# Kernel tuning notes

Hardware: AMD Instinct MI355X
Metric: run time of the kernel (lower is better)

Reference implementation:

```python
import jax, jax.numpy as jnp
import numpy as np

B, T, D, H, E = 8, 4096, 128, 4, 65536
O = D // H
NEG_SLOPE = 0.2

def setup_inputs() -> dict:
    key = jax.random.key(0)
    ks = jax.random.split(key, 5)
    s = 1.0 / np.sqrt(D)
    return {
        "x": jax.random.normal(ks[0], (B, T, D), jnp.float32),
        "edge_index": jax.random.randint(ks[1], (2, E), 0, T, jnp.int64),
        "W": jax.random.normal(ks[2], (D, H * O), jnp.float32) * s,
        "att_src": jax.random.normal(ks[3], (H, O), jnp.float32) * s,
        "att_dst": jax.random.normal(ks[4], (H, O), jnp.float32) * s,
        "bias": jnp.zeros((H * O,), jnp.float32),
    }

def reference(x, edge_index, W, att_src, att_dst, bias):
    b, t, d = x.shape
    N = b * t
    # linear projection of all nodes: [N, H, O]
    h = (x.reshape(N, d) @ W).reshape(N, H, O)
    # tile edge_index across batch with node offsets b_idx * t (matches repeat(1, b) + offsets)
    e = edge_index.shape[1]
    offsets = jnp.repeat(jnp.arange(b, dtype=edge_index.dtype), e) * t
    src = jnp.tile(edge_index[0], b) + offsets
    dst = jnp.tile(edge_index[1], b) + offsets
    # PyG GATConv default: add self loops over all N nodes
    loop = jnp.arange(N, dtype=edge_index.dtype)
    src = jnp.concatenate([src, loop])
    dst = jnp.concatenate([dst, loop])
    # per-node attention logits [N, H]
    a_src = jnp.sum(h * att_src, axis=-1)
    a_dst = jnp.sum(h * att_dst, axis=-1)
    # per-edge attention, softmax over incoming edges of each dst node
    alpha = jax.nn.leaky_relu(a_src[src] + a_dst[dst], NEG_SLOPE)  # [Et, H]
    amax = jax.ops.segment_max(jax.lax.stop_gradient(alpha), dst, num_segments=N)
    ealpha = jnp.exp(alpha - amax[dst])
    denom = jax.ops.segment_sum(ealpha, dst, num_segments=N)
    alpha = ealpha / (denom[dst] + 1e-16)
    # weighted scatter-aggregate of source features
    msg = h[src] * alpha[:, :, None]  # [Et, H, O]
    out = jax.ops.segment_sum(msg, dst, num_segments=N)  # [N, H, O]
    out = out.reshape(N, H * O) + bias
    return out.reshape(b, t, d)
```

## Files before the change

### kernel.cpp

```cpp
#include <hip/hip_runtime.h>

#define BATCH    8
#define T_LEN    4096
#define D_DIM    128
#define H_HEADS  4
#define O_DIM    32
#define E_EDGES  65536
#define N_NODES  (BATCH * T_LEN)
#define NEG_SLOPE 0.2f
#define ELLCAP   64
#define SPILLCAP 8192
#define GEMM_BLOCKS 512

typedef __attribute__((ext_vector_type(8))) short short8;
typedef __attribute__((ext_vector_type(4))) float f32x4;

__device__ __forceinline__ unsigned int bf16b(float f) {
    unsigned int u = __float_as_uint(f);
    u += 0x7FFFu + ((u >> 16) & 1u);
    return u >> 16;
}
__device__ __forceinline__ unsigned int bf16pack(float lo, float hi) {
    return bf16b(lo) | (bf16b(hi) << 16);
}
__device__ __forceinline__ float bf16f(unsigned short u) {
    return __uint_as_float((unsigned int)u << 16);
}

__device__ __forceinline__ int detect_shift(const int* ei, int tidx, int* s_sh) {
    if (tidx < 64) {
        const int nz = (ei[2 * tidx + 1] != 0) ? 1 : 0;
        const unsigned long long b = __ballot(nz);
        if (tidx == 0) *s_sh = (b == 0ull) ? 1 : 0;
    }
    __syncthreads();
    return *s_sh;
}

__launch_bounds__(256)
__global__ void prep_kernel(const float* __restrict__ W,
                            int* __restrict__ cnt,
                            unsigned short* __restrict__ WtG) {
    const int g = blockIdx.x * 256 + threadIdx.x;
    if (g < T_LEN + 1) cnt[g] = 0;
    const int i = g - 4352;
    if (i >= 0 && i < 128 * 128) {
        const int k   = i >> 7;
        const int col = i & 127;
        WtG[col * 128 + k] = (unsigned short)bf16b(W[k * 128 + col]);
    }
}

__launch_bounds__(256)
__global__ void gemm_ell_kernel(const float* __restrict__ x,
                                const unsigned short* __restrict__ WtG,
                                const float* __restrict__ attS,
                                const float* __restrict__ attD,
                                const int* __restrict__ ei,
                                unsigned short* __restrict__ hb,
                                float* __restrict__ aS,
                                float* __restrict__ aD,
                                int* __restrict__ cnt,
                                int* __restrict__ ell,
                                int* __restrict__ spill_cnt,
                                int2* __restrict__ spill) {
    __shared__ short Xb[64][136];
    __shared__ short Wt[128][136];
    __shared__ int   s_sh;

    const int tid = threadIdx.x;

    if (blockIdx.x >= GEMM_BLOCKS) {
        const int sh = detect_shift(ei, tid, &s_sh);
        const int j  = (blockIdx.x - GEMM_BLOCKS) * 256 + tid;
        const int s  = ei[j << sh];
        const int d  = ei[(E_EDGES + j) << sh];
        const int p  = atomicAdd(&cnt[d], 1);
        if (p < ELLCAP) {
            ell[d * ELLCAP + p] = s;
        } else {
            const int q = atomicAdd(spill_cnt, 1);
            if (q < SPILLCAP) spill[q] = make_int2(s, d);
        }
        return;
    }

    const int row0 = (blockIdx.x & 7) * T_LEN + ((blockIdx.x >> 3) << 6);

    const float4* X4 = (const float4*)(x + (size_t)row0 * 128);
    #pragma unroll
    for (int i = 0; i < 8; ++i) {
        const int idx = tid + 256 * i;
        const int row = idx >> 5;
        const int c4  = (idx & 31) * 4;
        const float4 v = X4[idx];
        uint2 u;
        u.x = bf16pack(v.x, v.y);
        u.y = bf16pack(v.z, v.w);
        *(uint2*)&Xb[row][c4] = u;
    }

    #pragma unroll
    for (int i = 0; i < 8; ++i) {
        const int idx = tid + 256 * i;
        const int row = idx >> 4;
        const int off = (idx & 15) * 8;
        *(short8*)&Wt[row][off] = *(const short8*)&WtG[row * 128 + off];
    }
    __syncthreads();

    const int wv    = tid >> 6;
    const int l     = tid & 63;
    const int lr    = l & 15;
    const int lg    = l >> 4;
    const int wrow0 = wv * 16;

    f32x4 acc[8];
    #pragma unroll
    for (int cf = 0; cf < 8; ++cf) acc[cf] = (f32x4){0.f, 0.f, 0.f, 0.f};

    #pragma unroll
    for (int kt = 0; kt < 4; ++kt) {
        const int k0 = kt * 32 + lg * 8;
        const short8 a = *(const short8*)&Xb[wrow0 + lr][k0];
        #pragma unroll
        for (int cf = 0; cf < 8; ++cf) {
            const short8 b = *(const short8*)&Wt[cf * 16 + lr][k0];
            acc[cf] = __builtin_amdgcn_mfma_f32_16x16x32_bf16(a, b, acc[cf], 0, 0, 0);
        }
    }

    #pragma unroll
    for (int cf = 0; cf < 8; ++cf) {
        #pragma unroll
        for (int r = 0; r < 4; ++r) {
            const int row = row0 + wrow0 + lg * 4 + r;
            hb[(size_t)row * 128 + cf * 16 + lr] = (unsigned short)bf16b(acc[cf][r]);
        }
    }

    float psr[4][4];
    float pdr[4][4];
    #pragma unroll
    for (int r = 0; r < 4; ++r)
        #pragma unroll
        for (int hd = 0; hd < 4; ++hd) { psr[r][hd] = 0.f; pdr[r][hd] = 0.f; }

    #pragma unroll
    for (int cf = 0; cf < 8; ++cf) {
        const float aSc = attS[cf * 16 + lr];
        const float aDc = attD[cf * 16 + lr];
        const int   hd  = cf >> 1;
        #pragma unroll
        for (int r = 0; r < 4; ++r) {
            psr[r][hd] += acc[cf][r] * aSc;
            pdr[r][hd] += acc[cf][r] * aDc;
        }
    }
    #pragma unroll
    for (int r = 0; r < 4; ++r)
        #pragma unroll
        for (int hd = 0; hd < 4; ++hd)
            #pragma unroll
            for (int off = 1; off < 16; off <<= 1) {
                psr[r][hd] += __shfl_xor(psr[r][hd], off);
                pdr[r][hd] += __shfl_xor(pdr[r][hd], off);
            }
    if (lr == 0) {
        #pragma unroll
        for (int r = 0; r < 4; ++r) {
            const int row = row0 + wrow0 + lg * 4 + r;
            *(float4*)&aS[(size_t)row * 4] =
                make_float4(psr[r][0], psr[r][1], psr[r][2], psr[r][3]);
            *(float4*)&aD[(size_t)row * 4] =
                make_float4(pdr[r][0], pdr[r][1], pdr[r][2], pdr[r][3]);
        }
    }
}

__launch_bounds__(256)
__global__ void gather_kernel(const int* __restrict__ cnt,
                              const int* __restrict__ ell,
                              const int* __restrict__ spill_cnt,
                              const int2* __restrict__ spill,
                              const unsigned short* __restrict__ hb,
                              const float* __restrict__ aS,
                              const float* __restrict__ aD,
                              const float* __restrict__ bias,
                              float* __restrict__ out) {
    __shared__ int   sbuf[4][ELLCAP + 1];
    __shared__ float wbuf[4][ELLCAP + 1][4];

    const int batch = blockIdx.x & 7;
    const int wv    = threadIdx.x >> 6;
    const int nib   = ((blockIdx.x >> 3) << 2) + wv;
    const int lane  = threadIdx.x & 63;
    const int base  = batch * T_LEN;
    const int n     = base + nib;

    const int deg = cnt[nib];
    const int m   = (deg < ELLCAP) ? deg : ELLCAP;

    const float4 ad4 = *(const float4*)(aD + (size_t)n * 4);

    if (lane < m) {
        const int s = ell[nib * ELLCAP + lane] + base;
        const float4 as4 = *(const float4*)(aS + (size_t)s * 4);
        float4 l;
        l.x = as4.x + ad4.x; l.x = (l.x > 0.f) ? l.x : NEG_SLOPE * l.x;
        l.y = as4.y + ad4.y; l.y = (l.y > 0.f) ? l.y : NEG_SLOPE * l.y;
        l.z = as4.z + ad4.z; l.z = (l.z > 0.f) ? l.z : NEG_SLOPE * l.z;
        l.w = as4.w + ad4.w; l.w = (l.w > 0.f) ? l.w : NEG_SLOPE * l.w;
        sbuf[wv][lane]    = s;
        wbuf[wv][lane][0] = __expf(l.x);
        wbuf[wv][lane][1] = __expf(l.y);
        wbuf[wv][lane][2] = __expf(l.z);
        wbuf[wv][lane][3] = __expf(l.w);
    }
    if (lane == (m & 63)) {
        const float4 as4 = *(const float4*)(aS + (size_t)n * 4);
        float4 l;
        l.x = as4.x + ad4.x; l.x = (l.x > 0.f) ? l.x : NEG_SLOPE * l.x;
        l.y = as4.y + ad4.y; l.y = (l.y > 0.f) ? l.y : NEG_SLOPE * l.y;
        l.z = as4.z + ad4.z; l.z = (l.z > 0.f) ? l.z : NEG_SLOPE * l.z;
        l.w = as4.w + ad4.w; l.w = (l.w > 0.f) ? l.w : NEG_SLOPE * l.w;
        sbuf[wv][m]    = n;
        wbuf[wv][m][0] = __expf(l.x);
        wbuf[wv][m][1] = __expf(l.y);
        wbuf[wv][m][2] = __expf(l.z);
        wbuf[wv][m][3] = __expf(l.w);
    }

    const int half = lane >> 5;
    const int li   = lane & 31;
    const int ci   = li * 4;
    const int hh   = li >> 3;

    float4 A = make_float4(0.f, 0.f, 0.f, 0.f);
    float dsum = 0.f;
    const int nst = m + 1;
    #pragma unroll 4
    for (int j = half; j < nst; j += 2) {
        const int   s = sbuf[wv][j];
        const float w = wbuf[wv][j][hh];
        dsum += w;
        const ushort4 hv = *(const ushort4*)(hb + (size_t)s * 128 + ci);
        A.x += w * bf16f(hv.x);
        A.y += w * bf16f(hv.y);
        A.z += w * bf16f(hv.z);
        A.w += w * bf16f(hv.w);
    }

    int sc = *spill_cnt;
    if (sc > 0 && half == 0) {
        if (sc > SPILLCAP) sc = SPILLCAP;
        const float adh = aD[(size_t)n * 4 + hh];
        for (int q = 0; q < sc; ++q) {
            const int2 e = spill[q];
            if (e.y == nib) {
                const int s = e.x + base;
                float l = aS[(size_t)s * 4 + hh] + adh;
                l = (l > 0.f) ? l : NEG_SLOPE * l;
                const float w = __expf(l);
                dsum += w;
                const ushort4 hv = *(const ushort4*)(hb + (size_t)s * 128 + ci);
                A.x += w * bf16f(hv.x);
                A.y += w * bf16f(hv.y);
                A.z += w * bf16f(hv.z);
                A.w += w * bf16f(hv.w);
            }
        }
    }

    A.x += __shfl_xor(A.x, 32);
    A.y += __shfl_xor(A.y, 32);
    A.z += __shfl_xor(A.z, 32);
    A.w += __shfl_xor(A.w, 32);
    dsum += __shfl_xor(dsum, 32);

    if (half == 0) {
        const float inv = 1.0f / (dsum + 1e-16f);
        const float4 b = *(const float4*)(bias + ci);
        float4 o;
        o.x = A.x * inv + b.x;
        o.y = A.y * inv + b.y;
        o.z = A.z * inv + b.z;
        o.w = A.w * inv + b.w;
        *(float4*)(out + (size_t)n * 128 + ci) = o;
    }
}

extern "C" void kernel_launch(void* const* d_in, const int* in_sizes, int n_in,
                              void* d_out, int out_size, void* d_ws, size_t ws_size,
                              hipStream_t stream) {
    const float* x    = (const float*)d_in[0];
    const int*   ei   = (const int*)  d_in[1];
    const float* W    = (const float*)d_in[2];
    const float* attS = (const float*)d_in[3];
    const float* attD = (const float*)d_in[4];
    const float* bias = (const float*)d_in[5];
    float* out = (float*)d_out;

    float* ws = (float*)d_ws;
    unsigned short* hb  = (unsigned short*)ws;
    float* aS           = ws + (size_t)N_NODES * 64;
    float* aD           = aS + (size_t)N_NODES * 4;
    unsigned short* WtG = (unsigned short*)(aD + (size_t)N_NODES * 4);
    int*   cnt          = (int*)(WtG + 128 * 128);
    int*   spill_cnt    = cnt + T_LEN;
    int*   ell          = spill_cnt + 2;
    int2*  spill        = (int2*)(ell + T_LEN * ELLCAP);

    prep_kernel<<<81, 256, 0, stream>>>(W, cnt, WtG);

    gemm_ell_kernel<<<GEMM_BLOCKS + 256, 256, 0, stream>>>(
        x, WtG, attS, attD, ei, hb, aS, aD, cnt, ell, spill_cnt, spill);

    gather_kernel<<<N_NODES / 4, 256, 0, stream>>>(cnt, ell, spill_cnt, spill,
                                                   hb, aS, aD, bias, out);
}
```

Before: 42.62 us.

## Map one destination node per half-wave in gather kernel with 1024-thread blocks

The gather kernel now assigns each 32-lane half-wave its own destination node, so a 64-lane wave handles two nodes instead of splitting one node's edges across its halves. This removes the cross-half shuffle reduction and the idle half during the output store. Blocks grow to 1024 threads covering 32 nodes each. Each half-wave now loops over all of its node's edges serially, and edge-weight setup loops in steps of 32. Divergence between the two nodes in a wave, and the larger block's shared memory and register limits, may reduce occupancy.

Measured after the change: 40.81 us. 1.04x faster.

```diff
diff --git a/kernel.cpp b/kernel.cpp
--- a/kernel.cpp
+++ b/kernel.cpp
@@ -178,7 +178,7 @@
     }
 }
 
-__launch_bounds__(256)
+__launch_bounds__(1024)
 __global__ void gather_kernel(const int* __restrict__ cnt,
                               const int* __restrict__ ell,
                               const int* __restrict__ spill_cnt,
@@ -188,14 +188,16 @@
                               const float* __restrict__ aD,
                               const float* __restrict__ bias,
                               float* __restrict__ out) {
-    __shared__ int   sbuf[4][ELLCAP + 1];
-    __shared__ float wbuf[4][ELLCAP + 1][4];
+    __shared__ int   sbuf[16][2][ELLCAP + 1];
+    __shared__ float wbuf[16][2][ELLCAP + 1][4];
 
     const int batch = blockIdx.x & 7;
     const int wv    = threadIdx.x >> 6;
-    const int nib   = ((blockIdx.x >> 3) << 2) + wv;
     const int lane  = threadIdx.x & 63;
+    const int half  = lane >> 5;
+    const int li    = lane & 31;
     const int base  = batch * T_LEN;
+    const int nib   = ((blockIdx.x >> 3) << 5) + (wv << 1) + half;
     const int n     = base + nib;
 
     const int deg = cnt[nib];
@@ -203,46 +205,44 @@
 
     const float4 ad4 = *(const float4*)(aD + (size_t)n * 4);
 
-    if (lane < m) {
-        const int s = ell[nib * ELLCAP + lane] + base;
+    if (li == 0) {
+        const float4 as4 = *(const float4*)(aS + (size_t)n * 4);
+        float4 l;
+        l.x = as4.x + ad4.x; l.x = (l.x > 0.f) ? l.x : NEG_SLOPE * l.x;
+        l.y = as4.y + ad4.y; l.y = (l.y > 0.f) ? l.y : NEG_SLOPE * l.y;
+        l.z = as4.z + ad4.z; l.z = (l.z > 0.f) ? l.z : NEG_SLOPE * l.z;
+        l.w = as4.w + ad4.w; l.w = (l.w > 0.f) ? l.w : NEG_SLOPE * l.w;
+        sbuf[wv][half][0]    = n;
+        wbuf[wv][half][0][0] = __expf(l.x);
+        wbuf[wv][half][0][1] = __expf(l.y);
+        wbuf[wv][half][0][2] = __expf(l.z);
+        wbuf[wv][half][0][3] = __expf(l.w);
+    }
+    for (int jj = li; jj < m; jj += 32) {
+        const int s = ell[nib * ELLCAP + jj] + base;
         const float4 as4 = *(const float4*)(aS + (size_t)s * 4);
         float4 l;
         l.x = as4.x + ad4.x; l.x = (l.x > 0.f) ? l.x : NEG_SLOPE * l.x;
         l.y = as4.y + ad4.y; l.y = (l.y > 0.f) ? l.y : NEG_SLOPE * l.y;
         l.z = as4.z + ad4.z; l.z = (l.z > 0.f) ? l.z : NEG_SLOPE * l.z;
         l.w = as4.w + ad4.w; l.w = (l.w > 0.f) ? l.w : NEG_SLOPE * l.w;
-        sbuf[wv][lane]    = s;
-        wbuf[wv][lane][0] = __expf(l.x);
-        wbuf[wv][lane][1] = __expf(l.y);
-        wbuf[wv][lane][2] = __expf(l.z);
-        wbuf[wv][lane][3] = __expf(l.w);
-    }
-    if (lane == (m & 63)) {
-        const float4 as4 = *(const float4*)(aS + (size_t)n * 4);
-        float4 l;
-        l.x = as4.x + ad4.x; l.x = (l.x > 0.f) ? l.x : NEG_SLOPE * l.x;
-        l.y = as4.y + ad4.y; l.y = (l.y > 0.f) ? l.y : NEG_SLOPE * l.y;
-        l.z = as4.z + ad4.z; l.z = (l.z > 0.f) ? l.z : NEG_SLOPE * l.z;
-        l.w = as4.w + ad4.w; l.w = (l.w > 0.f) ? l.w : NEG_SLOPE * l.w;
-        sbuf[wv][m]    = n;
-        wbuf[wv][m][0] = __expf(l.x);
-        wbuf[wv][m][1] = __expf(l.y);
-        wbuf[wv][m][2] = __expf(l.z);
-        wbuf[wv][m][3] = __expf(l.w);
-    }
-
-    const int half = lane >> 5;
-    const int li   = lane & 31;
-    const int ci   = li * 4;
-    const int hh   = li >> 3;
+        sbuf[wv][half][jj + 1]    = s;
+        wbuf[wv][half][jj + 1][0] = __expf(l.x);
+        wbuf[wv][half][jj + 1][1] = __expf(l.y);
+        wbuf[wv][half][jj + 1][2] = __expf(l.z);
+        wbuf[wv][half][jj + 1][3] = __expf(l.w);
+    }
+
+    const int ci = li * 4;
+    const int hh = li >> 3;
 
     float4 A = make_float4(0.f, 0.f, 0.f, 0.f);
     float dsum = 0.f;
     const int nst = m + 1;
     #pragma unroll 4
-    for (int j = half; j < nst; j += 2) {
-        const int   s = sbuf[wv][j];
-        const float w = wbuf[wv][j][hh];
+    for (int j = 0; j < nst; ++j) {
+        const int   s = sbuf[wv][half][j];
+        const float w = wbuf[wv][half][j][hh];
         dsum += w;
         const ushort4 hv = *(const ushort4*)(hb + (size_t)s * 128 + ci);
         A.x += w * bf16f(hv.x);
@@ -252,9 +252,10 @@
     }
 
     int sc = *spill_cnt;
-    if (sc > 0 && half == 0) {
+    if (sc > 0) {
         if (sc > SPILLCAP) sc = SPILLCAP;
-        const float adh = aD[(size_t)n * 4 + hh];
+        const float adh = (hh == 0) ? ad4.x : (hh == 1) ? ad4.y
+                        : (hh == 2) ? ad4.z : ad4.w;
         for (int q = 0; q < sc; ++q) {
             const int2 e = spill[q];
             if (e.y == nib) {
@@ -272,22 +273,14 @@
         }
     }
 
-    A.x += __shfl_xor(A.x, 32);
-    A.y += __shfl_xor(A.y, 32);
-    A.z += __shfl_xor(A.z, 32);
-    A.w += __shfl_xor(A.w, 32);
-    dsum += __shfl_xor(dsum, 32);
-
-    if (half == 0) {
-        const float inv = 1.0f / (dsum + 1e-16f);
-        const float4 b = *(const float4*)(bias + ci);
-        float4 o;
-        o.x = A.x * inv + b.x;
-        o.y = A.y * inv + b.y;
-        o.z = A.z * inv + b.z;
-        o.w = A.w * inv + b.w;
-        *(float4*)(out + (size_t)n * 128 + ci) = o;
-    }
+    const float inv = 1.0f / (dsum + 1e-16f);
+    const float4 b = *(const float4*)(bias + ci);
+    float4 o;
+    o.x = A.x * inv + b.x;
+    o.y = A.y * inv + b.y;
+    o.z = A.z * inv + b.z;
+    o.w = A.w * inv + b.w;
+    *(float4*)(out + (size_t)n * 128 + ci) = o;
 }
 
 extern "C" void kernel_launch(void* const* d_in, const int* in_sizes, int n_in,
@@ -316,6 +309,6 @@
     gemm_ell_kernel<<<GEMM_BLOCKS + 256, 256, 0, stream>>>(
         x, WtG, attS, attD, ei, hb, aS, aD, cnt, ell, spill_cnt, spill);
 
-    gather_kernel<<<N_NODES / 4, 256, 0, stream>>>(cnt, ell, spill_cnt, spill,
-                                                   hb, aS, aD, bias, out);
-}
+    gather_kernel<<<N_NODES / 32, 1024, 0, stream>>>(cnt, ell, spill_cnt, spill,
+                                                     hb, aS, aD, bias, out);
+}
```
